# Optimization experiments

Measured on AMD Instinct MI355X. Metric: run time of the kernel, lower is better.

Reference implementation:

```python
import jax, jax.numpy as jnp
import numpy as np

NHID = 768
H = 128        # LSTM hidden per direction
NHEADS = 6
NDIR = 12      # 6 heads x 2 directions; first 6 = forward, last 6 = backward
DFF = 4 * NHID
CAT = 2 * H * NHEADS  # 1536


def setup_inputs() -> dict:
    key = jax.random.key(0)
    ks = jax.random.split(key, 12)
    s = 0.05
    return {
        "embeddings": jax.random.normal(ks[0], (16, 512, NHID), jnp.float32),
        # stacked LSTM params; gate order i,f,g,o as in PyTorch
        "W_ih": jax.random.normal(ks[1], (NDIR, 4 * H, NHID), jnp.float32) * s,
        "W_hh": jax.random.normal(ks[2], (NDIR, 4 * H, H), jnp.float32) * s,
        "b_ih": jax.random.normal(ks[3], (NDIR, 4 * H), jnp.float32) * s,
        "b_hh": jax.random.normal(ks[4], (NDIR, 4 * H), jnp.float32) * s,
        "W_int": jax.random.normal(ks[5], (DFF, CAT), jnp.float32) * s,
        "b_int": jax.random.normal(ks[6], (DFF,), jnp.float32) * s,
        "W_out": jax.random.normal(ks[7], (NHID, DFF), jnp.float32) * s,
        "b_out": jax.random.normal(ks[8], (NHID,), jnp.float32) * s,
        "gamma": jnp.ones((NHID,), jnp.float32),
        "beta": jnp.zeros((NHID,), jnp.float32),
    }


def _multi_bilstm(x, W_ih, W_hh, b_ih, b_hh):
    # x: [B,S,D] -> concat of 6 bidirectional LSTM outputs [B,S,1536]
    B, S, _ = x.shape
    # input projections for all 12 directions at once: [12,B,S,4H]
    xp = jnp.einsum('bsd,kgd->kbsg', x, W_ih) + (b_ih + b_hh)[:, None, None, :]
    # reverse time for the 6 backward directions
    xp = jnp.concatenate([xp[:NHEADS], xp[NHEADS:, :, ::-1]], axis=0)
    xs = jnp.moveaxis(xp, 2, 0)  # [S,12,B,4H]

    def step(carry, z_x):
        h, c = carry  # each [12,B,H]
        z = z_x + jnp.einsum('kbh,kgh->kbg', h, W_hh)
        i, f, g, o = jnp.split(z, 4, axis=-1)
        c = jax.nn.sigmoid(f) * c + jax.nn.sigmoid(i) * jnp.tanh(g)
        h = jax.nn.sigmoid(o) * jnp.tanh(c)
        return (h, c), h

    init = (jnp.zeros((NDIR, B, H), x.dtype), jnp.zeros((NDIR, B, H), x.dtype))
    _, ys = jax.lax.scan(step, init, xs)        # [S,12,B,H]
    ys = jnp.moveaxis(ys, 0, 2)                 # [12,B,S,H]
    ys = jnp.concatenate([ys[:NHEADS], ys[NHEADS:, :, ::-1]], axis=0)
    # per-head layout: head0_fwd, head0_bwd, head1_fwd, ... (matches torch.cat of per-LSTM outputs)
    ys = ys.reshape(2, NHEADS, B, S, H).transpose(2, 3, 1, 0, 4)
    return ys.reshape(B, S, CAT)


def reference(embeddings, W_ih, W_hh, b_ih, b_hh, W_int, b_int, W_out, b_out, gamma, beta):
    cat = _multi_bilstm(embeddings, W_ih, W_hh, b_ih, b_hh)
    inter = jax.nn.gelu(cat @ W_int.T + b_int, approximate=False)
    proj = inter @ W_out.T + b_out
    res = embeddings + proj  # dropout is identity (p=0 / eval)
    mu = jnp.mean(res, axis=-1, keepdims=True)
    var = jnp.mean(jnp.square(res - mu), axis=-1, keepdims=True)
    return (res - mu) * jax.lax.rsqrt(var + 1e-5) * gamma + beta
```

## Files before the change

kernel.cpp:

```cpp
#include <hip/hip_runtime.h>

typedef __attribute__((ext_vector_type(4))) float f32x4;
typedef __attribute__((ext_vector_type(8))) short short8;
typedef unsigned short u16;
typedef unsigned int u32;

__device__ __forceinline__ u16 f2bf(float f){
  u32 x = __float_as_uint(f);
  u32 r = x + 0x7fffu + ((x >> 16) & 1u);
  return (u16)(r >> 16);
}
__device__ __forceinline__ float bf2f32(u32 u){ return __uint_as_float(u << 16); }

__device__ __forceinline__ void gld_lds16(const u16* g, u16* l){
  __builtin_amdgcn_global_load_lds((const __attribute__((address_space(1))) void*)g,
                                   (__attribute__((address_space(3))) void*)l, 16, 0, 0);
}

__device__ __forceinline__ f32x4 mfma16(short8 a, short8 b, f32x4 c){
  return __builtin_amdgcn_mfma_f32_16x16x32_bf16(a, b, c, 0, 0, 0);
}

__device__ __forceinline__ float sigf(float x){
  return __builtin_amdgcn_rcpf(1.0f + __expf(-x));
}
__device__ __forceinline__ float tanhf_(float x){
  float e = __expf(2.0f * x);
  return 1.0f - 2.0f * __builtin_amdgcn_rcpf(e + 1.0f);
}

__global__ __launch_bounds__(256) void k_castall(const float* __restrict__ s0, const float* __restrict__ s1,
                          const float* __restrict__ s2, const float* __restrict__ s3,
                          const float* __restrict__ s4,
                          u16* __restrict__ d0, u16* __restrict__ d1, u16* __restrict__ d2,
                          u16* __restrict__ d3, u16* __restrict__ d4)
{
  int i = blockIdx.x * 256 + threadIdx.x;
  const float* s; u16* d; int off;
  if (i < 1572864)      { s = s0; d = d0; off = i; }
  else if (i < 2752512) { s = s1; d = d1; off = i - 1572864; }
  else if (i < 2949120) { s = s2; d = d2; off = i - 2752512; }
  else if (i < 4128768) { s = s3; d = d3; off = i - 2949120; }
  else                  { s = s4; d = d4; off = i - 4128768; }
  float4 v = ((const float4*)s)[off];
  ushort4 o; o.x=f2bf(v.x); o.y=f2bf(v.y); o.z=f2bf(v.z); o.w=f2bf(v.w);
  ((ushort4*)d)[off] = o;
}

template<int MODE>
__global__ __launch_bounds__(256) void k_gemm(const u16* __restrict__ A, const u16* __restrict__ B,
                       void* __restrict__ C, void* __restrict__ C2,
                       const float* __restrict__ bias1, const float* __restrict__ bias2,
                       int M, int N, int K, int lda)
{
  __shared__ __align__(16) u16 lA[128*64];
  __shared__ __align__(16) u16 lB[128*64];
  int nwg = gridDim.x;
  int bid = blockIdx.x;
  int half = 0;
  if (MODE == 2){
    int h2 = nwg >> 1;
    half = (bid >= h2) ? 1 : 0;
    bid -= half ? h2 : 0;
    nwg = h2;
  }
  int koff = half * K;
  int nbm = M >> 7;
  int q = nwg >> 3;
  int swz = (bid & 7) * q + (bid >> 3);
  int bm = swz % nbm, bn = swz / nbm;
  int tid = threadIdx.x, lane = tid & 63;
  int wv = tid >> 6;
  int wrow = (wv & 1) << 6, wcol = (wv >> 1) << 6;
  int l15 = lane & 15, lhi = lane >> 4;
  const u16* Ag = A + (size_t)bm * 128 * lda + koff;
  const u16* Bg = B + (size_t)bn * 128 * lda + koff;
  f32x4 acc[4][4];
  #pragma unroll
  for (int i=0;i<4;++i)
    #pragma unroll
    for(int j=0;j<4;++j) acc[i][j] = (f32x4){0.f,0.f,0.f,0.f};

  for (int k0 = 0; k0 < K; k0 += 64){
    #pragma unroll
    for (int i = 0; i < 4; ++i){
      int c = i*256 + tid;
      int row = c >> 3, col8 = (c & 7) << 3;
      gld_lds16(Ag + (size_t)row*lda + k0 + col8, &lA[c<<3]);
      gld_lds16(Bg + (size_t)row*lda + k0 + col8, &lB[c<<3]);
    }
    __syncthreads();
    #pragma unroll
    for (int kk = 0; kk < 2; ++kk){
      short8 af[4], bfr[4];
      #pragma unroll
      for (int f = 0; f < 4; ++f)
        af[f] = *(const short8*)&lA[(wrow + f*16 + l15)*64 + kk*32 + lhi*8];
      #pragma unroll
      for (int g = 0; g < 4; ++g)
        bfr[g] = *(const short8*)&lB[(wcol + g*16 + l15)*64 + kk*32 + lhi*8];
      #pragma unroll
      for (int f = 0; f < 4; ++f)
        #pragma unroll
        for (int g = 0; g < 4; ++g)
          acc[f][g] = mfma16(af[f], bfr[g], acc[f][g]);
    }
    __syncthreads();
  }
  #pragma unroll
  for (int f = 0; f < 4; ++f){
    #pragma unroll
    for (int r = 0; r < 4; ++r){
      int m = bm*128 + wrow + f*16 + lhi*4 + r;
      #pragma unroll
      for (int g = 0; g < 4; ++g){
        int n = bn*128 + wcol + g*16 + l15;
        float v = acc[f][g][r];
        if (MODE == 0){
          v += bias1[n] + bias2[n];
          ((u16*)C)[(size_t)m * N + n] = f2bf(v);
        } else if (MODE == 1){
          v += bias1[n];
          v = 0.5f * v * (1.0f + erff(v * 0.70710678118f));
          ((u16*)C)[(size_t)m * N + n] = f2bf(v);
        } else {
          if (!half) v += bias1[n];
          ((float*)(half ? C2 : C))[(size_t)m * N + n] = v;
        }
      }
    }
  }
}

__global__ __launch_bounds__(512) void k_scan(const u16* __restrict__ whh, const u16* __restrict__ xp,
                       u16* __restrict__ cat)
{
  __shared__ __align__(16) u16 hb[2][4*144];
  int bid = blockIdx.x;
  int d = bid >> 2, bg = bid & 3;
  int tid = threadIdx.x, lane = tid & 63, w = tid >> 6;
  int l15 = lane & 15, lhi = lane >> 4;

  u16* hbf = (u16*)hb;
  for (int i = tid; i < 2*4*144; i += 512) hbf[i] = 0;

  short8 wf[4][4];
  #pragma unroll
  for (int g = 0; g < 4; ++g)
    #pragma unroll
    for (int kk = 0; kk < 4; ++kk)
      wf[g][kk] = *(const short8*)(whh + ((size_t)d*512 + g*128 + w*16 + l15)*128 + kk*32 + lhi*8);

  int b = bg*4 + lhi;
  int dim = w*16 + l15;
  bool fwd = (d < 6);
  const u16* zrow = xp + (size_t)b*512*6144 + d*512 + dim;

  u32 Zi[4], Zf[4], Zg[4], Zo[4];
  #pragma unroll
  for (int j = 0; j < 4; ++j){
    int s = fwd ? j : 511 - j;
    const u16* p = zrow + (size_t)s*6144;
    Zi[j] = p[0]; Zf[j] = p[128]; Zg[j] = p[256]; Zo[j] = p[384];
  }

  f32x4 a0={0.f,0.f,0.f,0.f}, a1=a0, a2=a0, a3=a0;
  float cr = 0.f;
  int head = fwd ? d : d - 6;
  int posoff = fwd ? 0 : 128;
  size_t catlane = (size_t)b*512*1536 + head*256 + posoff + dim;
  int catoff = fwd ? 0 : 511*1536;
  int catstep = fwd ? 1536 : -1536;

  int hrd = (l15 >> 2)*144 + lhi*8;
  int hwr = lhi*144 + dim;

  __syncthreads();

#define SCAN_STEP(T, RB, WB, S)                                                \
  {                                                                            \
    short8 hf0 = *(const short8*)&hb[RB][hrd + 0*32];                          \
    short8 hf1 = *(const short8*)&hb[RB][hrd + 1*32];                          \
    short8 hf2 = *(const short8*)&hb[RB][hrd + 2*32];                          \
    short8 hf3 = *(const short8*)&hb[RB][hrd + 3*32];                          \
    a0[0] = bf2f32(Zi[S]); a1[0] = bf2f32(Zf[S]);                              \
    a2[0] = bf2f32(Zg[S]); a3[0] = bf2f32(Zo[S]);                              \
    int t4 = (T) + 4; if (t4 > 511) t4 = 511;                                  \
    int s4 = fwd ? t4 : 511 - t4;                                              \
    const u16* pf = zrow + (size_t)s4*6144;                                    \
    Zi[S] = pf[0]; Zf[S] = pf[128]; Zg[S] = pf[256]; Zo[S] = pf[384];          \
               \
    a2 = mfma16(hf0, wf[2][0], a2); a0 = mfma16(hf0, wf[0][0], a0);            \
    a1 = mfma16(hf0, wf[1][0], a1); a3 = mfma16(hf0, wf[3][0], a3);            \
    a2 = mfma16(hf1, wf[2][1], a2); a0 = mfma16(hf1, wf[0][1], a0);            \
    a1 = mfma16(hf1, wf[1][1], a1); a3 = mfma16(hf1, wf[3][1], a3);            \
    a2 = mfma16(hf2, wf[2][2], a2); a0 = mfma16(hf2, wf[0][2], a0);            \
    a1 = mfma16(hf2, wf[1][2], a1); a3 = mfma16(hf2, wf[3][2], a3);            \
    a2 = mfma16(hf3, wf[2][3], a2); a0 = mfma16(hf3, wf[0][3], a0);            \
    a1 = mfma16(hf3, wf[1][3], a1); a3 = mfma16(hf3, wf[3][3], a3);            \
    float tg = tanhf_(a2[0]);                                                  \
    float fi = sigf(a0[0]), ff = sigf(a1[0]), fo = sigf(a3[0]);                \
    cr = ff*cr + fi*tg;                                                        \
    float hv = fo * tanhf_(cr);                                                \
    u32 hp32;                                                                  \
    asm("v_cvt_pk_bf16_f32 %0, %1, %2" : "=v"(hp32) : "v"(hv), "v"(hv));       \
    u16 hp = (u16)hp32;                                                        \
    hb[WB][hwr] = hp;                                                          \
    asm volatile("s_waitcnt lgkmcnt(0)" ::: "memory");                         \
    __builtin_amdgcn_s_barrier();                                              \
    cat[catlane + catoff] = hp;                                                \
    catoff += catstep;                                                         \
  }

  for (int t = 0; t < 512; t += 4){
    SCAN_STEP(t,   0, 1, 0)
    SCAN_STEP(t+1, 1, 0, 1)
    SCAN_STEP(t+2, 0, 1, 2)
    SCAN_STEP(t+3, 1, 0, 3)
  }
#undef SCAN_STEP
}

__global__ __launch_bounds__(256) void k_ln(const float* __restrict__ emb, const float* __restrict__ p0,
                     const float* __restrict__ p1,
                     const float* __restrict__ gamma, const float* __restrict__ beta,
                     float* __restrict__ out)
{
  int row = blockIdx.x, tid = threadIdx.x;
  const float* pe = emb + (size_t)row * 768;
  const float* pa = p0 + (size_t)row * 768;
  const float* pb = p1 + (size_t)row * 768;
  float v0 = pe[tid]     + pa[tid]     + pb[tid];
  float v1 = pe[tid+256] + pa[tid+256] + pb[tid+256];
  float v2 = pe[tid+512] + pa[tid+512] + pb[tid+512];
  float s = v0+v1+v2, s2 = v0*v0+v1*v1+v2*v2;
  #pragma unroll
  for (int o = 32; o > 0; o >>= 1){ s += __shfl_down(s, o); s2 += __shfl_down(s2, o); }
  __shared__ float rs[4], rq[4];
  int wv = tid >> 6;
  if ((tid & 63) == 0){ rs[wv] = s; rq[wv] = s2; }
  __syncthreads();
  s = rs[0]+rs[1]+rs[2]+rs[3];
  s2 = rq[0]+rq[1]+rq[2]+rq[3];
  float mu = s * (1.0f/768.0f);
  float var = s2 * (1.0f/768.0f) - mu*mu;
  float rr = rsqrtf(var + 1e-5f);
  float* po = out + (size_t)row * 768;
  po[tid]     = (v0-mu)*rr*gamma[tid]     + beta[tid];
  po[tid+256] = (v1-mu)*rr*gamma[tid+256] + beta[tid+256];
  po[tid+512] = (v2-mu)*rr*gamma[tid+512] + beta[tid+512];
}

extern "C" void kernel_launch(void* const* d_in, const int* in_sizes, int n_in,
                              void* d_out, int out_size, void* d_ws, size_t ws_size,
                              hipStream_t stream)
{
  const float* emb   = (const float*)d_in[0];
  const float* W_ih  = (const float*)d_in[1];
  const float* W_hh  = (const float*)d_in[2];
  const float* b_ih  = (const float*)d_in[3];
  const float* b_hh  = (const float*)d_in[4];
  const float* W_int = (const float*)d_in[5];
  const float* b_int = (const float*)d_in[6];
  const float* W_out = (const float*)d_in[7];
  const float* b_out = (const float*)d_in[8];
  const float* gamma = (const float*)d_in[9];
  const float* beta  = (const float*)d_in[10];
  float* out = (float*)d_out;

  char* ws = (char*)d_ws;
  u16* embb  = (u16*)(ws + 0);
  u16* wihb  = (u16*)(ws + 12582912);
  u16* whhb  = (u16*)(ws + 22020096);
  u16* wintb = (u16*)(ws + 23592960);
  u16* woutb = (u16*)(ws + 33030144);
  u16* catb  = (u16*)(ws + 37748736);
  float* proj1=(float*)(ws + 37748736);
  u16* xp    = (u16*)(ws + 62914560);
  u16* interb= (u16*)(ws + 62914560);
  float* proj0=(float*)(ws + 113246208);

  hipLaunchKernelGGL(k_castall, dim3(18432), dim3(256), 0, stream,
                     emb, W_ih, W_hh, W_int, W_out, embb, wihb, whhb, wintb, woutb);

  hipLaunchKernelGGL((k_gemm<0>), dim3(3072), dim3(256), 0, stream,
                     embb, wihb, (void*)xp, nullptr, b_ih, b_hh, 8192, 6144, 768, 768);
  hipLaunchKernelGGL(k_scan, dim3(48), dim3(512), 0, stream, whhb, xp, catb);
  hipLaunchKernelGGL((k_gemm<1>), dim3(1536), dim3(256), 0, stream,
                     catb, wintb, (void*)interb, nullptr, b_int, nullptr, 8192, 3072, 1536, 1536);
  hipLaunchKernelGGL((k_gemm<2>), dim3(768), dim3(256), 0, stream,
                     interb, woutb, (void*)proj0, (void*)proj1, b_out, nullptr, 8192, 768, 1536, 3072);
  hipLaunchKernelGGL(k_ln, dim3(8192), dim3(256), 0, stream, emb, proj0, proj1, gamma, beta, out);
}
```

Baseline: 598.9 us.

## Add 256x256 double-buffered swizzled GEMM kernel for input and intermediate projections

Adds a new GEMM kernel with 256x256 tiles, 512 threads, double-buffered LDS fed by direct global-to-LDS loads, an XOR-swizzled LDS layout, and MFMA priority raising. It replaces the 128x128 single-buffered GEMM for the LSTM input projection and the GELU intermediate GEMM. The goal is more data reuse per tile, fewer LDS bank conflicts, and overlap of the next tile's loads with the current compute. The output GEMM stays on the old kernel, now specialised as k_gemm2. Larger tiles give fewer workgroups, which may hurt load balance across CUs, and use much more LDS and registers.

Measured after the change: 541.3 us. 1.11x faster.

```diff
diff --git a/kernel.cpp b/kernel.cpp
--- a/kernel.cpp
+++ b/kernel.cpp
@@ -48,22 +48,144 @@
 }
 
 template<int MODE>
-__global__ __launch_bounds__(256) void k_gemm(const u16* __restrict__ A, const u16* __restrict__ B,
-                       void* __restrict__ C, void* __restrict__ C2,
-                       const float* __restrict__ bias1, const float* __restrict__ bias2,
+__global__ __launch_bounds__(512, 2) void k_gemm256(
+    const u16* __restrict__ A, const u16* __restrict__ B, void* __restrict__ C,
+    const float* __restrict__ bias1, const float* __restrict__ bias2,
+    int M, int N, int K, int lda)
+{
+  __shared__ __align__(16) u16 lA[2][256*64];
+  __shared__ __align__(16) u16 lB[2][256*64];
+  int nwg = gridDim.x;
+  int bid = blockIdx.x;
+  int q = nwg >> 3;
+  int swz = (bid & 7) * q + (bid >> 3);
+  int nbm = M >> 8;
+  int bm = swz % nbm, bn = swz / nbm;
+  int tid = threadIdx.x, lane = tid & 63;
+  int wv = tid >> 6;
+  int wm = wv & 1, wn = wv >> 1;
+  int l15 = lane & 15, lhi = lane >> 4;
+  const u16* Ag = A + (size_t)(bm << 8) * lda;
+  const u16* Bg = B + (size_t)(bn << 8) * lda;
+
+  int srow[4], ssl[4];
+  #pragma unroll
+  for (int i = 0; i < 4; ++i){
+    int c = i*512 + tid;
+    srow[i] = c >> 3;
+    ssl[i] = (((c & 7) ^ (srow[i] & 7)) << 3);
+  }
+  int axr = l15 & 7;
+  int aoff0 = (wm*128 + l15)*64 + ((lhi    ) ^ axr)*8;
+  int aoff1 = (wm*128 + l15)*64 + ((lhi + 4) ^ axr)*8;
+  int boff0 = (wn*64  + l15)*64 + ((lhi    ) ^ axr)*8;
+  int boff1 = (wn*64  + l15)*64 + ((lhi + 4) ^ axr)*8;
+
+  f32x4 acc[8][4];
+  #pragma unroll
+  for (int i = 0; i < 8; ++i)
+    #pragma unroll
+    for (int j = 0; j < 4; ++j)
+      acc[i][j] = (f32x4){0.f,0.f,0.f,0.f};
+
+  int NT = K >> 6;
+
+  #pragma unroll
+  for (int i = 0; i < 4; ++i)
+    gld_lds16(Ag + (size_t)srow[i]*lda + ssl[i], &lA[0][(i*512+tid)*8]);
+  #pragma unroll
+  for (int i = 0; i < 4; ++i)
+    gld_lds16(Bg + (size_t)srow[i]*lda + ssl[i], &lB[0][(i*512+tid)*8]);
+  asm volatile("s_waitcnt vmcnt(0)" ::: "memory");
+  __builtin_amdgcn_s_barrier();
+
+  for (int t = 0; t < NT; ++t){
+    int bp = t & 1;
+    const u16* sA = lA[bp];
+    const u16* sB = lB[bp];
+    u16* dA = lA[bp^1];
+    u16* dB = lB[bp^1];
+    int k1 = (t + 1) << 6;
+    bool more = (t + 1 < NT);
+    short8 bf[4][2];
+    #pragma unroll
+    for (int p = 0; p < 4; ++p){
+      if (p == 0){
+        #pragma unroll
+        for (int ni = 0; ni < 4; ++ni){
+          bf[ni][0] = *(const short8*)&sB[boff0 + ni*1024];
+          bf[ni][1] = *(const short8*)&sB[boff1 + ni*1024];
+        }
+      }
+      short8 a00 = *(const short8*)&sA[aoff0 + (2*p)*1024];
+      short8 a01 = *(const short8*)&sA[aoff1 + (2*p)*1024];
+      short8 a10 = *(const short8*)&sA[aoff0 + (2*p+1)*1024];
+      short8 a11 = *(const short8*)&sA[aoff1 + (2*p+1)*1024];
+      if (more && p == 0){
+        #pragma unroll
+        for (int i = 0; i < 4; ++i)
+          gld_lds16(Ag + (size_t)srow[i]*lda + k1 + ssl[i], &dA[(i*512+tid)*8]);
+      }
+      if (more && p == 1){
+        #pragma unroll
+        for (int i = 0; i < 4; ++i)
+          gld_lds16(Bg + (size_t)srow[i]*lda + k1 + ssl[i], &dB[(i*512+tid)*8]);
+      }
+      __builtin_amdgcn_s_barrier();
+      asm volatile("s_waitcnt lgkmcnt(0)" ::: "memory");
+      __builtin_amdgcn_sched_barrier(0);
+      __builtin_amdgcn_s_setprio(1);
+      #pragma unroll
+      for (int ni = 0; ni < 4; ++ni){
+        acc[2*p  ][ni] = mfma16(a00, bf[ni][0], acc[2*p  ][ni]);
+        acc[2*p  ][ni] = mfma16(a01, bf[ni][1], acc[2*p  ][ni]);
+        acc[2*p+1][ni] = mfma16(a10, bf[ni][0], acc[2*p+1][ni]);
+        acc[2*p+1][ni] = mfma16(a11, bf[ni][1], acc[2*p+1][ni]);
+      }
+      __builtin_amdgcn_s_setprio(0);
+      if (p == 3){
+        asm volatile("s_waitcnt vmcnt(0)" ::: "memory");
+      }
+      __builtin_amdgcn_s_barrier();
+    }
+  }
+
+  float bsum[4];
+  #pragma unroll
+  for (int ni = 0; ni < 4; ++ni){
+    int n = (bn << 8) + wn*64 + ni*16 + l15;
+    bsum[ni] = (MODE == 0) ? (bias1[n] + bias2[n]) : bias1[n];
+  }
+  #pragma unroll
+  for (int mi = 0; mi < 8; ++mi){
+    #pragma unroll
+    for (int r = 0; r < 4; ++r){
+      int m = (bm << 8) + wm*128 + mi*16 + lhi*4 + r;
+      #pragma unroll
+      for (int ni = 0; ni < 4; ++ni){
+        int n = (bn << 8) + wn*64 + ni*16 + l15;
+        float v = acc[mi][ni][r] + bsum[ni];
+        if (MODE == 1)
+          v = 0.5f * v * (1.0f + erff(v * 0.70710678118f));
+        ((u16*)C)[(size_t)m * N + n] = f2bf(v);
+      }
+    }
+  }
+}
+
+__global__ __launch_bounds__(256) void k_gemm2(const u16* __restrict__ A, const u16* __restrict__ B,
+                       float* __restrict__ C, float* __restrict__ C2,
+                       const float* __restrict__ bias1,
                        int M, int N, int K, int lda)
 {
   __shared__ __align__(16) u16 lA[128*64];
   __shared__ __align__(16) u16 lB[128*64];
   int nwg = gridDim.x;
   int bid = blockIdx.x;
-  int half = 0;
-  if (MODE == 2){
-    int h2 = nwg >> 1;
-    half = (bid >= h2) ? 1 : 0;
-    bid -= half ? h2 : 0;
-    nwg = h2;
-  }
+  int h2 = nwg >> 1;
+  int half = (bid >= h2) ? 1 : 0;
+  bid -= half ? h2 : 0;
+  nwg = h2;
   int koff = half * K;
   int nbm = M >> 7;
   int q = nwg >> 3;
@@ -107,6 +229,7 @@
     }
     __syncthreads();
   }
+  float* Cw = half ? C2 : C;
   #pragma unroll
   for (int f = 0; f < 4; ++f){
     #pragma unroll
@@ -116,17 +239,8 @@
       for (int g = 0; g < 4; ++g){
         int n = bn*128 + wcol + g*16 + l15;
         float v = acc[f][g][r];
-        if (MODE == 0){
-          v += bias1[n] + bias2[n];
-          ((u16*)C)[(size_t)m * N + n] = f2bf(v);
-        } else if (MODE == 1){
-          v += bias1[n];
-          v = 0.5f * v * (1.0f + erff(v * 0.70710678118f));
-          ((u16*)C)[(size_t)m * N + n] = f2bf(v);
-        } else {
-          if (!half) v += bias1[n];
-          ((float*)(half ? C2 : C))[(size_t)m * N + n] = v;
-        }
+        if (!half) v += bias1[n];
+        Cw[(size_t)m * N + n] = v;
       }
     }
   }
@@ -189,7 +303,6 @@
     int s4 = fwd ? t4 : 511 - t4;                                              \
     const u16* pf = zrow + (size_t)s4*6144;                                    \
     Zi[S] = pf[0]; Zf[S] = pf[128]; Zg[S] = pf[256]; Zo[S] = pf[384];          \
-               \
     a2 = mfma16(hf0, wf[2][0], a2); a0 = mfma16(hf0, wf[0][0], a0);            \
     a1 = mfma16(hf0, wf[1][0], a1); a3 = mfma16(hf0, wf[3][0], a3);            \
     a2 = mfma16(hf1, wf[2][1], a2); a0 = mfma16(hf1, wf[0][1], a0);            \
@@ -283,12 +396,12 @@
   hipLaunchKernelGGL(k_castall, dim3(18432), dim3(256), 0, stream,
                      emb, W_ih, W_hh, W_int, W_out, embb, wihb, whhb, wintb, woutb);
 
-  hipLaunchKernelGGL((k_gemm<0>), dim3(3072), dim3(256), 0, stream,
-                     embb, wihb, (void*)xp, nullptr, b_ih, b_hh, 8192, 6144, 768, 768);
+  hipLaunchKernelGGL((k_gemm256<0>), dim3(768), dim3(512), 0, stream,
+                     embb, wihb, (void*)xp, b_ih, b_hh, 8192, 6144, 768, 768);
   hipLaunchKernelGGL(k_scan, dim3(48), dim3(512), 0, stream, whhb, xp, catb);
-  hipLaunchKernelGGL((k_gemm<1>), dim3(1536), dim3(256), 0, stream,
-                     catb, wintb, (void*)interb, nullptr, b_int, nullptr, 8192, 3072, 1536, 1536);
-  hipLaunchKernelGGL((k_gemm<2>), dim3(768), dim3(256), 0, stream,
-                     interb, woutb, (void*)proj0, (void*)proj1, b_out, nullptr, 8192, 768, 1536, 3072);
+  hipLaunchKernelGGL((k_gemm256<1>), dim3(384), dim3(512), 0, stream,
+                     catb, wintb, (void*)interb, b_int, nullptr, 8192, 3072, 1536, 1536);
+  hipLaunchKernelGGL(k_gemm2, dim3(768), dim3(256), 0, stream,
+                     interb, woutb, proj0, proj1, b_out, 8192, 768, 1536, 3072);
   hipLaunchKernelGGL(k_ln, dim3(8192), dim3(256), 0, stream, emb, proj0, proj1, gamma, beta, out);
 }
```

## Replace GEMMs with 256x192 pipelined swizzled-LDS kernel and interleave W_ih gates

Applied to the files above, without the earlier changes.

The 128x128 single-buffered GEMM is replaced by a 512-thread kernel with 256x192 tiles. It double-buffers A and triple-buffers B in LDS, uses an XOR-swizzled LDS layout, and overlaps global-to-LDS loads with MFMA through phase barriers and setprio. W_ih rows are permuted so the four gates of each hidden unit sit next to each other, which lets the scan load i,f,g,o as one ushort4 instead of four strided scalars. The risks are higher register and LDS use per block and fewer workgroups, which may hurt the smaller GEMMs.

Measured after the change: 506.1 us. 1.18x faster.

```diff
diff --git a/kernel.cpp b/kernel.cpp
--- a/kernel.cpp
+++ b/kernel.cpp
@@ -31,30 +31,39 @@
 
 __global__ __launch_bounds__(256) void k_castall(const float* __restrict__ s0, const float* __restrict__ s1,
                           const float* __restrict__ s2, const float* __restrict__ s3,
-                          const float* __restrict__ s4,
                           u16* __restrict__ d0, u16* __restrict__ d1, u16* __restrict__ d2,
-                          u16* __restrict__ d3, u16* __restrict__ d4)
+                          u16* __restrict__ d3)
 {
   int i = blockIdx.x * 256 + threadIdx.x;
   const float* s; u16* d; int off;
   if (i < 1572864)      { s = s0; d = d0; off = i; }
-  else if (i < 2752512) { s = s1; d = d1; off = i - 1572864; }
-  else if (i < 2949120) { s = s2; d = d2; off = i - 2752512; }
-  else if (i < 4128768) { s = s3; d = d3; off = i - 2949120; }
-  else                  { s = s4; d = d4; off = i - 4128768; }
+  else if (i < 1769472) { s = s1; d = d1; off = i - 1572864; }
+  else if (i < 2949120) { s = s2; d = d2; off = i - 1769472; }
+  else                  { s = s3; d = d3; off = i - 2949120; }
   float4 v = ((const float4*)s)[off];
   ushort4 o; o.x=f2bf(v.x); o.y=f2bf(v.y); o.z=f2bf(v.z); o.w=f2bf(v.w);
   ((ushort4*)d)[off] = o;
 }
 
+__global__ __launch_bounds__(192) void k_permw(const float* __restrict__ wih, u16* __restrict__ dst)
+{
+  int np = blockIdx.x;
+  int d = np >> 9, r = np & 511;
+  int src = d*512 + (r & 3)*128 + (r >> 2);
+  float4 v = ((const float4*)(wih + (size_t)src*768))[threadIdx.x];
+  ushort4 o; o.x=f2bf(v.x); o.y=f2bf(v.y); o.z=f2bf(v.z); o.w=f2bf(v.w);
+  ((ushort4*)(dst + (size_t)np*768))[threadIdx.x] = o;
+}
+
 template<int MODE>
-__global__ __launch_bounds__(256) void k_gemm(const u16* __restrict__ A, const u16* __restrict__ B,
-                       void* __restrict__ C, void* __restrict__ C2,
-                       const float* __restrict__ bias1, const float* __restrict__ bias2,
-                       int M, int N, int K, int lda)
-{
-  __shared__ __align__(16) u16 lA[128*64];
-  __shared__ __align__(16) u16 lB[128*64];
+__global__ __launch_bounds__(512) void k_gemm3(
+    const u16* __restrict__ A, const u16* __restrict__ B,
+    void* __restrict__ C, void* __restrict__ C2,
+    const float* __restrict__ bias1, const float* __restrict__ bias2,
+    int M, int N, int K, int lda)
+{
+  __shared__ __align__(16) u16 lA[2][256*64];
+  __shared__ __align__(16) u16 lB[3][192*64];
   int nwg = gridDim.x;
   int bid = blockIdx.x;
   int half = 0;
@@ -65,67 +74,134 @@
     nwg = h2;
   }
   int koff = half * K;
-  int nbm = M >> 7;
   int q = nwg >> 3;
   int swz = (bid & 7) * q + (bid >> 3);
-  int bm = swz % nbm, bn = swz / nbm;
+  int nbn = N / 192;
+  int grp = nbn << 3;
+  int gid = swz / grp, rem = swz % grp;
+  int bm = (gid << 3) + (rem & 7), bn = rem >> 3;
   int tid = threadIdx.x, lane = tid & 63;
   int wv = tid >> 6;
-  int wrow = (wv & 1) << 6, wcol = (wv >> 1) << 6;
+  int wm = wv & 1, wn = wv >> 1;
   int l15 = lane & 15, lhi = lane >> 4;
-  const u16* Ag = A + (size_t)bm * 128 * lda + koff;
-  const u16* Bg = B + (size_t)bn * 128 * lda + koff;
-  f32x4 acc[4][4];
-  #pragma unroll
-  for (int i=0;i<4;++i)
+  const u16* Ag = A + (size_t)(bm << 8) * lda + koff;
+  const u16* Bg = B + (size_t)(bn * 192) * lda + koff;
+
+  int srA[4], slA[4];
+  #pragma unroll
+  for (int i = 0; i < 4; ++i){
+    int c = i*512 + tid;
+    srA[i] = c >> 3;
+    slA[i] = (((c & 7) ^ (srA[i] & 7)) << 3);
+  }
+  int srB[3], slB[3];
+  #pragma unroll
+  for (int i = 0; i < 3; ++i){
+    int c = i*512 + tid;
+    srB[i] = c >> 3;
+    slB[i] = (((c & 7) ^ (srB[i] & 7)) << 3);
+  }
+  int axr = l15 & 7;
+  int aoff0 = (wm*128 + l15)*64 + ((lhi    ) ^ axr)*8;
+  int aoff1 = (wm*128 + l15)*64 + ((lhi + 4) ^ axr)*8;
+  int boff0 = (wn*48  + l15)*64 + ((lhi    ) ^ axr)*8;
+  int boff1 = (wn*48  + l15)*64 + ((lhi + 4) ^ axr)*8;
+
+  f32x4 acc[8][3];
+  #pragma unroll
+  for (int i = 0; i < 8; ++i)
     #pragma unroll
-    for(int j=0;j<4;++j) acc[i][j] = (f32x4){0.f,0.f,0.f,0.f};
-
-  for (int k0 = 0; k0 < K; k0 += 64){
+    for (int j = 0; j < 3; ++j)
+      acc[i][j] = (f32x4){0.f,0.f,0.f,0.f};
+
+  int NT = K >> 6;
+
+#define STAGE_A(TT)                                                            \
+  { int ko = (TT) << 6; u16* dA = lA[(TT) & 1];                                \
+    _Pragma("unroll")                                                          \
+    for (int i = 0; i < 4; ++i)                                                \
+      gld_lds16(Ag + (size_t)srA[i]*lda + ko + slA[i], &dA[(i*512+tid)*8]); }
+#define STAGE_B(TT)                                                            \
+  { int ko = (TT) << 6; u16* dB = lB[(TT) % 3];                                \
+    _Pragma("unroll")                                                          \
+    for (int i = 0; i < 3; ++i)                                                \
+      gld_lds16(Bg + (size_t)srB[i]*lda + ko + slB[i], &dB[(i*512+tid)*8]); }
+
+  STAGE_A(0)
+  STAGE_B(0)
+  STAGE_B(1)
+  asm volatile("s_waitcnt vmcnt(3)" ::: "memory");
+  __builtin_amdgcn_s_barrier();
+
+  for (int t = 0; t < NT; ++t){
+    const u16* sA = lA[t & 1];
+    const u16* sB = lB[t % 3];
+    short8 bf[3][2];
     #pragma unroll
-    for (int i = 0; i < 4; ++i){
-      int c = i*256 + tid;
-      int row = c >> 3, col8 = (c & 7) << 3;
-      gld_lds16(Ag + (size_t)row*lda + k0 + col8, &lA[c<<3]);
-      gld_lds16(Bg + (size_t)row*lda + k0 + col8, &lB[c<<3]);
+    for (int p = 0; p < 4; ++p){
+      if (p == 0){
+        #pragma unroll
+        for (int ni = 0; ni < 3; ++ni){
+          bf[ni][0] = *(const short8*)&sB[boff0 + ni*1024];
+          bf[ni][1] = *(const short8*)&sB[boff1 + ni*1024];
+        }
+      }
+      short8 a00 = *(const short8*)&sA[aoff0 + (2*p)*1024];
+      short8 a01 = *(const short8*)&sA[aoff1 + (2*p)*1024];
+      short8 a10 = *(const short8*)&sA[aoff0 + (2*p+1)*1024];
+      short8 a11 = *(const short8*)&sA[aoff1 + (2*p+1)*1024];
+      if (p == 0 && t + 1 < NT){ STAGE_A(t+1) }
+      if (p == 1 && t + 2 < NT){ STAGE_B(t+2) }
+      __builtin_amdgcn_s_barrier();
+      asm volatile("s_waitcnt lgkmcnt(0)" ::: "memory");
+      __builtin_amdgcn_sched_barrier(0);
+      __builtin_amdgcn_s_setprio(1);
+      #pragma unroll
+      for (int ni = 0; ni < 3; ++ni){
+        acc[2*p  ][ni] = mfma16(a00, bf[ni][0], acc[2*p  ][ni]);
+        acc[2*p  ][ni] = mfma16(a01, bf[ni][1], acc[2*p  ][ni]);
+        acc[2*p+1][ni] = mfma16(a10, bf[ni][0], acc[2*p+1][ni]);
+        acc[2*p+1][ni] = mfma16(a11, bf[ni][1], acc[2*p+1][ni]);
+      }
+      __builtin_amdgcn_s_setprio(0);
+      if (p == 3){
+        if (t + 2 < NT){
+          asm volatile("s_waitcnt vmcnt(3)" ::: "memory");
+        } else if (t + 1 < NT){
+          asm volatile("s_waitcnt vmcnt(0)" ::: "memory");
+        }
+      }
+      __builtin_amdgcn_s_barrier();
     }
-    __syncthreads();
+  }
+#undef STAGE_A
+#undef STAGE_B
+
+  #pragma unroll
+  for (int ni = 0; ni < 3; ++ni){
+    int n = bn*192 + wn*48 + ni*16 + l15;
+    float bs;
+    if (MODE == 0){
+      int d = n >> 9, r = n & 511;
+      int src = d*512 + (r & 3)*128 + (r >> 2);
+      bs = bias1[src] + bias2[src];
+    } else {
+      bs = bias1[n];
+    }
     #pragma unroll
-    for (int kk = 0; kk < 2; ++kk){
-      short8 af[4], bfr[4];
+    for (int mi = 0; mi < 8; ++mi){
       #pragma unroll
-      for (int f = 0; f < 4; ++f)
-        af[f] = *(const short8*)&lA[(wrow + f*16 + l15)*64 + kk*32 + lhi*8];
-      #pragma unroll
-      for (int g = 0; g < 4; ++g)
-        bfr[g] = *(const short8*)&lB[(wcol + g*16 + l15)*64 + kk*32 + lhi*8];
-      #pragma unroll
-      for (int f = 0; f < 4; ++f)
-        #pragma unroll
-        for (int g = 0; g < 4; ++g)
-          acc[f][g] = mfma16(af[f], bfr[g], acc[f][g]);
-    }
-    __syncthreads();
-  }
-  #pragma unroll
-  for (int f = 0; f < 4; ++f){
-    #pragma unroll
-    for (int r = 0; r < 4; ++r){
-      int m = bm*128 + wrow + f*16 + lhi*4 + r;
-      #pragma unroll
-      for (int g = 0; g < 4; ++g){
-        int n = bn*128 + wcol + g*16 + l15;
-        float v = acc[f][g][r];
-        if (MODE == 0){
-          v += bias1[n] + bias2[n];
+      for (int r = 0; r < 4; ++r){
+        int m = (bm << 8) + wm*128 + mi*16 + lhi*4 + r;
+        float v = acc[mi][ni][r];
+        if (MODE == 2){
+          if (!half) v += bs;
+          ((float*)(half ? C2 : C))[(size_t)m * N + n] = v;
+        } else {
+          v += bs;
+          if (MODE == 1)
+            v = 0.5f * v * (1.0f + erff(v * 0.70710678118f));
           ((u16*)C)[(size_t)m * N + n] = f2bf(v);
-        } else if (MODE == 1){
-          v += bias1[n];
-          v = 0.5f * v * (1.0f + erff(v * 0.70710678118f));
-          ((u16*)C)[(size_t)m * N + n] = f2bf(v);
-        } else {
-          if (!half) v += bias1[n];
-          ((float*)(half ? C2 : C))[(size_t)m * N + n] = v;
         }
       }
     }
@@ -154,14 +230,13 @@
   int b = bg*4 + lhi;
   int dim = w*16 + l15;
   bool fwd = (d < 6);
-  const u16* zrow = xp + (size_t)b*512*6144 + d*512 + dim;
-
-  u32 Zi[4], Zf[4], Zg[4], Zo[4];
+  const u16* zbase = xp + (size_t)b*512*6144 + d*512 + dim*4;
+
+  ushort4 Z[4];
   #pragma unroll
   for (int j = 0; j < 4; ++j){
     int s = fwd ? j : 511 - j;
-    const u16* p = zrow + (size_t)s*6144;
-    Zi[j] = p[0]; Zf[j] = p[128]; Zg[j] = p[256]; Zo[j] = p[384];
+    Z[j] = *(const ushort4*)(zbase + (size_t)s*6144);
   }
 
   f32x4 a0={0.f,0.f,0.f,0.f}, a1=a0, a2=a0, a3=a0;
@@ -183,13 +258,11 @@
     short8 hf1 = *(const short8*)&hb[RB][hrd + 1*32];                          \
     short8 hf2 = *(const short8*)&hb[RB][hrd + 2*32];                          \
     short8 hf3 = *(const short8*)&hb[RB][hrd + 3*32];                          \
-    a0[0] = bf2f32(Zi[S]); a1[0] = bf2f32(Zf[S]);                              \
-    a2[0] = bf2f32(Zg[S]); a3[0] = bf2f32(Zo[S]);                              \
+    a0[0] = bf2f32((u32)Z[S].x); a1[0] = bf2f32((u32)Z[S].y);                  \
+    a2[0] = bf2f32((u32)Z[S].z); a3[0] = bf2f32((u32)Z[S].w);                  \
     int t4 = (T) + 4; if (t4 > 511) t4 = 511;                                  \
     int s4 = fwd ? t4 : 511 - t4;                                              \
-    const u16* pf = zrow + (size_t)s4*6144;                                    \
-    Zi[S] = pf[0]; Zf[S] = pf[128]; Zg[S] = pf[256]; Zo[S] = pf[384];          \
-               \
+    Z[S] = *(const ushort4*)(zbase + (size_t)s4*6144);                         \
     a2 = mfma16(hf0, wf[2][0], a2); a0 = mfma16(hf0, wf[0][0], a0);            \
     a1 = mfma16(hf0, wf[1][0], a1); a3 = mfma16(hf0, wf[3][0], a3);            \
     a2 = mfma16(hf1, wf[2][1], a2); a0 = mfma16(hf1, wf[0][1], a0);            \
@@ -280,15 +353,16 @@
   u16* interb= (u16*)(ws + 62914560);
   float* proj0=(float*)(ws + 113246208);
 
-  hipLaunchKernelGGL(k_castall, dim3(18432), dim3(256), 0, stream,
-                     emb, W_ih, W_hh, W_int, W_out, embb, wihb, whhb, wintb, woutb);
-
-  hipLaunchKernelGGL((k_gemm<0>), dim3(3072), dim3(256), 0, stream,
+  hipLaunchKernelGGL(k_castall, dim3(13824), dim3(256), 0, stream,
+                     emb, W_hh, W_int, W_out, embb, whhb, wintb, woutb);
+  hipLaunchKernelGGL(k_permw, dim3(6144), dim3(192), 0, stream, W_ih, wihb);
+
+  hipLaunchKernelGGL((k_gemm3<0>), dim3(1024), dim3(512), 0, stream,
                      embb, wihb, (void*)xp, nullptr, b_ih, b_hh, 8192, 6144, 768, 768);
   hipLaunchKernelGGL(k_scan, dim3(48), dim3(512), 0, stream, whhb, xp, catb);
-  hipLaunchKernelGGL((k_gemm<1>), dim3(1536), dim3(256), 0, stream,
+  hipLaunchKernelGGL((k_gemm3<1>), dim3(512), dim3(512), 0, stream,
                      catb, wintb, (void*)interb, nullptr, b_int, nullptr, 8192, 3072, 1536, 1536);
-  hipLaunchKernelGGL((k_gemm<2>), dim3(768), dim3(256), 0, stream,
+  hipLaunchKernelGGL((k_gemm3<2>), dim3(256), dim3(512), 0, stream,
                      interb, woutb, (void*)proj0, (void*)proj1, b_out, nullptr, 8192, 768, 1536, 3072);
   hipLaunchKernelGGL(k_ln, dim3(8192), dim3(256), 0, stream, emb, proj0, proj1, gamma, beta, out);
 }
```
